# Optimization experiments

Hardware: AMD Instinct MI355X
Metric: run time of the kernel (lower is better)

The kernel has to match this reference:

```python
import jax, jax.numpy as jnp
from jax import lax
import numpy as np

B, T, IN, H, OUT = 1024, 512, 64, 128, 2
BN_EPS = 1e-5


def _gru_layer(x, w_ih, w_hh, b_ih, b_hh):
    # x: [B, T, F]; w_ih: [3H, F]; w_hh: [3H, H]; gate order = (r, z, n) as in PyTorch
    Bb = x.shape[0]
    Hh = w_hh.shape[1]
    xg = jnp.einsum('btf,gf->btg', x, w_ih) + b_ih  # precompute input gates [B, T, 3H]

    def step(h, xg_t):
        hg = h @ w_hh.T + b_hh                       # [B, 3H]
        xr, xz, xn = jnp.split(xg_t, 3, axis=-1)
        hr, hz, hn = jnp.split(hg, 3, axis=-1)
        r = jax.nn.sigmoid(xr + hr)
        z = jax.nn.sigmoid(xz + hz)
        n = jnp.tanh(xn + r * hn)
        h_new = (1.0 - z) * n + z * h
        return h_new, h_new

    h0 = jnp.zeros((Bb, Hh), dtype=x.dtype)
    _, ys = lax.scan(step, h0, jnp.swapaxes(xg, 0, 1))  # scan over time
    return jnp.swapaxes(ys, 0, 1)                        # [B, T, H]


def setup_inputs() -> dict:
    key = jax.random.key(0)
    ks = jax.random.split(key, 16)
    s_in = 1.0 / np.sqrt(H)  # PyTorch GRU init scale
    d = {
        'x': jax.random.normal(ks[0], (B, T, IN), dtype=jnp.float32),
        'w_ih0': jax.random.uniform(ks[1], (3 * H, IN), minval=-s_in, maxval=s_in),
        'w_hh0': jax.random.uniform(ks[2], (3 * H, H), minval=-s_in, maxval=s_in),
        'b_ih0': jax.random.uniform(ks[3], (3 * H,), minval=-s_in, maxval=s_in),
        'b_hh0': jax.random.uniform(ks[4], (3 * H,), minval=-s_in, maxval=s_in),
        'w_ih1': jax.random.uniform(ks[5], (3 * H, H), minval=-s_in, maxval=s_in),
        'w_hh1': jax.random.uniform(ks[6], (3 * H, H), minval=-s_in, maxval=s_in),
        'b_ih1': jax.random.uniform(ks[7], (3 * H,), minval=-s_in, maxval=s_in),
        'b_hh1': jax.random.uniform(ks[8], (3 * H,), minval=-s_in, maxval=s_in),
        'fc1_w': jax.random.normal(ks[9], (H // 2, H)) * 0.05,
        'fc1_b': jnp.zeros((H // 2,)),
        'fc2_w': jax.random.normal(ks[10], (OUT, H // 2)) * 0.05,
        'fc2_b': jnp.zeros((OUT,)),
        'bn_gamma': jnp.ones((H // 2,)),
        'bn_beta': jnp.zeros((H // 2,)),
        'bn_mean': jnp.zeros((H // 2,)),
        'bn_var': jnp.ones((H // 2,)),
    }
    return d


def reference(x, w_ih0, w_hh0, b_ih0, b_hh0, w_ih1, w_hh1, b_ih1, b_hh1,
              fc1_w, fc1_b, fc2_w, fc2_b, bn_gamma, bn_beta, bn_mean, bn_var):
    h1 = _gru_layer(x, w_ih0, w_hh0, b_ih0, b_hh0)   # [B, T, H]
    h2 = _gru_layer(h1, w_ih1, w_hh1, b_ih1, b_hh1)  # [B, T, H]
    out = h2[:, -1, :]                                # last timestep [B, H]
    # dropout = identity (eval mode)
    out = jax.nn.relu(out @ fc1_w.T + fc1_b)          # [B, H/2]
    out = (out - bn_mean) * jax.lax.rsqrt(bn_var + BN_EPS) * bn_gamma + bn_beta
    out = out @ fc2_w.T + fc2_b                       # [B, 2]
    return out
```

## Files before the change

### kernel.cpp

```cpp
#include <hip/hip_runtime.h>
#include <hip/hip_bf16.h>

namespace {

typedef _Float16 h16;
typedef _Float16 f16x8 __attribute__((ext_vector_type(8)));
typedef _Float16 f16x4 __attribute__((ext_vector_type(4)));
typedef _Float16 f16x2 __attribute__((ext_vector_type(2)));
typedef float    f32x4 __attribute__((ext_vector_type(4)));
typedef unsigned long long u64;

constexpr int T_SEQ = 512;
constexpr int B_SZ  = 1024;
constexpr int H_DIM = 128;
constexpr int ROWS  = 16;
constexpr int NT    = 512;
constexpr int NGRP  = B_SZ / ROWS;
constexpr int CHUNK = 32;

template <int INDIM, bool PROD>
__device__ void gru_body(char* smem_raw,
                         const float* __restrict__ xin,
                         const float* __restrict__ w_ih,
                         const float* __restrict__ w_hh,
                         const float* __restrict__ b_ih,
                         const float* __restrict__ b_hh,
                         u64* __restrict__ h1q,
                         int* __restrict__ flag,
                         float* __restrict__ h2out,
                         const int g)
{
  constexpr int KSH  = H_DIM / 32;
  constexpr int KSX  = INDIM / 32;
  constexpr int ROWP = H_DIM + INDIM + 8;

  auto hx = reinterpret_cast<h16 (*)[ROWS][ROWP]>(smem_raw);

  const int tid = threadIdx.x;
  const int wv  = tid >> 6;
  const int ln  = tid & 63;
  const int q   = ln >> 4;
  const int lr  = ln & 15;
  const int r0  = g * ROWS;
  const int j0  = wv * 16 + q * 4;

  f16x8 wA[3][KSH], wB[3][KSX];
  #pragma unroll
  for (int p = 0; p < 3; ++p) {
    const int gr = p * H_DIM + wv * 16 + lr;
    #pragma unroll
    for (int ks = 0; ks < KSH; ++ks) {
      const float* pw = w_hh + (size_t)gr * H_DIM + ks * 32 + q * 8;
      const float4 v0 = *(const float4*)(pw);
      const float4 v1 = *(const float4*)(pw + 4);
      f16x8 f;
      f[0]=(h16)v0.x; f[1]=(h16)v0.y; f[2]=(h16)v0.z; f[3]=(h16)v0.w;
      f[4]=(h16)v1.x; f[5]=(h16)v1.y; f[6]=(h16)v1.z; f[7]=(h16)v1.w;
      wA[p][ks] = f;
    }
    #pragma unroll
    for (int ks = 0; ks < KSX; ++ks) {
      const float* pw = w_ih + (size_t)gr * INDIM + ks * 32 + q * 8;
      const float4 v0 = *(const float4*)(pw);
      const float4 v1 = *(const float4*)(pw + 4);
      f16x8 f;
      f[0]=(h16)v0.x; f[1]=(h16)v0.y; f[2]=(h16)v0.z; f[3]=(h16)v0.w;
      f[4]=(h16)v1.x; f[5]=(h16)v1.y; f[6]=(h16)v1.z; f[7]=(h16)v1.w;
      wB[p][ks] = f;
    }
  }

  f32x4 bR, bZ, bNx, bNh;
  {
    const float4 ir  = *(const float4*)&b_ih[j0];
    const float4 hr  = *(const float4*)&b_hh[j0];
    const float4 iz  = *(const float4*)&b_ih[H_DIM + j0];
    const float4 hz  = *(const float4*)&b_hh[H_DIM + j0];
    const float4 in_ = *(const float4*)&b_ih[2 * H_DIM + j0];
    const float4 hn  = *(const float4*)&b_hh[2 * H_DIM + j0];
    bR[0]=ir.x+hr.x; bR[1]=ir.y+hr.y; bR[2]=ir.z+hr.z; bR[3]=ir.w+hr.w;
    bZ[0]=iz.x+hz.x; bZ[1]=iz.y+hz.y; bZ[2]=iz.z+hz.z; bZ[3]=iz.w+hz.w;
    bNx[0]=in_.x; bNx[1]=in_.y; bNx[2]=in_.z; bNx[3]=in_.w;
    bNh[0]=hn.x;  bNh[1]=hn.y;  bNh[2]=hn.z;  bNh[3]=hn.w;
  }

  const int sr = tid >> 5;
  const int si = tid & 31;

  {
    f16x4 z; z[0]=z[1]=z[2]=z[3] = (h16)0.f;
    *(f16x4*)&hx[0][sr][si * 4] = z;
  }
  f16x4 h_old; h_old[0]=h_old[1]=h_old[2]=h_old[3] = (h16)0.f;

  f16x2 sA, sB;
  if constexpr (PROD) {
    const float2 v0 = *(const float2*)(xin + ((size_t)(r0 + sr) * T_SEQ + 0) * 64 + si * 2);
    f16x2 s0; s0[0] = (h16)v0.x; s0[1] = (h16)v0.y;
    *(f16x2*)&hx[0][sr][H_DIM + si * 2] = s0;
    const float2 v1 = *(const float2*)(xin + ((size_t)(r0 + sr) * T_SEQ + 1) * 64 + si * 2);
    sA[0] = (h16)v1.x; sA[1] = (h16)v1.y;
  } else {
    while (__hip_atomic_load(flag, __ATOMIC_ACQUIRE, __HIP_MEMORY_SCOPE_AGENT) < 1)
      __builtin_amdgcn_s_sleep(2);
    const u64 bits = __hip_atomic_load(&h1q[((size_t)0 * B_SZ + r0 + sr) * 32 + si],
                                       __ATOMIC_RELAXED, __HIP_MEMORY_SCOPE_AGENT);
    f16x4 s0; __builtin_memcpy(&s0, &bits, 8);
    *(f16x4*)&hx[0][sr][H_DIM + si * 4] = s0;
  }
  __syncthreads();

  auto gates = [&](const f32x4& aR, const f32x4& aZ, const f32x4& aNx2, const f32x4& aNh2,
                   f16x4& nv4, float* hnv) {
    #pragma unroll
    for (int i = 0; i < 4; ++i) {
      const float rg = __builtin_amdgcn_rcpf(1.f + __expf(-aR[i]));
      const float zg = __builtin_amdgcn_rcpf(1.f + __expf(-aZ[i]));
      const float na = aNx2[i] + rg * aNh2[i];
      const float e2 = __expf(2.f * na);
      const float ng = 1.f - 2.f * __builtin_amdgcn_rcpf(e2 + 1.f);
      const float ho = (float)h_old[i];
      const float hn = ng + zg * (ho - ng);
      hnv[i] = hn;
      nv4[i] = (h16)hn;
    }
    h_old = nv4;
  };

  if constexpr (PROD) {
    auto pstep = [&](int t, int cur, f16x2& s_use, f16x2& s_load) {
      f16x8 bh[KSH], bx[KSX];
      #pragma unroll
      for (int ks = 0; ks < KSH; ++ks) bh[ks] = *(const f16x8*)&hx[cur][lr][ks * 32 + q * 8];
      #pragma unroll
      for (int ks = 0; ks < KSX; ++ks) bx[ks] = *(const f16x8*)&hx[cur][lr][H_DIM + ks * 32 + q * 8];

      {
        const int tt = (t + 2 < T_SEQ) ? t + 2 : T_SEQ - 1;
        const float2 v = *(const float2*)(xin + ((size_t)(r0 + sr) * T_SEQ + tt) * 64 + si * 2);
        s_load[0] = (h16)v.x; s_load[1] = (h16)v.y;
      }

      f32x4 aR = bR, aZ = bZ, aNh2 = bNh, aNx2 = bNx;
      #pragma unroll
      for (int ks = 0; ks < KSH; ++ks) {
        aR   = __builtin_amdgcn_mfma_f32_16x16x32_f16(wA[0][ks], bh[ks], aR, 0, 0, 0);
        aZ   = __builtin_amdgcn_mfma_f32_16x16x32_f16(wA[1][ks], bh[ks], aZ, 0, 0, 0);
        aNh2 = __builtin_amdgcn_mfma_f32_16x16x32_f16(wA[2][ks], bh[ks], aNh2, 0, 0, 0);
      }
      #pragma unroll
      for (int ks = 0; ks < KSX; ++ks) {
        aR   = __builtin_amdgcn_mfma_f32_16x16x32_f16(wB[0][ks], bx[ks], aR, 0, 0, 0);
        aZ   = __builtin_amdgcn_mfma_f32_16x16x32_f16(wB[1][ks], bx[ks], aZ, 0, 0, 0);
        aNx2 = __builtin_amdgcn_mfma_f32_16x16x32_f16(wB[2][ks], bx[ks], aNx2, 0, 0, 0);
      }

      f16x4 nv4; float hnv[4];
      gates(aR, aZ, aNx2, aNh2, nv4, hnv);

      u64 bits; __builtin_memcpy(&bits, &nv4, 8);
      __hip_atomic_store(&h1q[((size_t)t * B_SZ + r0 + lr) * 32 + (j0 >> 2)], bits,
                         __ATOMIC_RELAXED, __HIP_MEMORY_SCOPE_AGENT);

      *(f16x4*)&hx[cur ^ 1][lr][j0] = nv4;
      *(f16x2*)&hx[cur ^ 1][sr][H_DIM + si * 2] = s_use;

      if ((t & (CHUNK - 1)) == CHUNK - 1) __threadfence();
      __syncthreads();
      if (((t & (CHUNK - 1)) == CHUNK - 1) && tid == 0)
        __hip_atomic_store(flag, (t + 1) >> 5, __ATOMIC_RELEASE, __HIP_MEMORY_SCOPE_AGENT);
    };

    #pragma unroll 1
    for (int t = 0; t < T_SEQ; t += 2) {
      pstep(t,     0, sA, sB);
      pstep(t + 1, 1, sB, sA);
    }
  } else {
    #pragma unroll 1
    for (int t = 0; t < T_SEQ; ++t) {
      const int cur = t & 1;
      f16x8 bh[KSH], bx[KSX];
      #pragma unroll
      for (int ks = 0; ks < KSH; ++ks) bh[ks] = *(const f16x8*)&hx[cur][lr][ks * 32 + q * 8];
      #pragma unroll
      for (int ks = 0; ks < KSX; ++ks) bx[ks] = *(const f16x8*)&hx[cur][lr][H_DIM + ks * 32 + q * 8];

      f16x4 sN;
      const bool have = (t + 1 < T_SEQ);
      if (have) {
        if (((t + 1) & (CHUNK - 1)) == 0) {
          const int need = ((t + 1) >> 5) + 1;
          while (__hip_atomic_load(flag, __ATOMIC_ACQUIRE, __HIP_MEMORY_SCOPE_AGENT) < need)
            __builtin_amdgcn_s_sleep(2);
        }
        const u64 bits = __hip_atomic_load(&h1q[((size_t)(t + 1) * B_SZ + r0 + sr) * 32 + si],
                                           __ATOMIC_RELAXED, __HIP_MEMORY_SCOPE_AGENT);
        __builtin_memcpy(&sN, &bits, 8);
      }

      f32x4 aR = bR, aZ = bZ, aNh2 = bNh, aNx2 = bNx;
      #pragma unroll
      for (int ks = 0; ks < KSH; ++ks) {
        aR   = __builtin_amdgcn_mfma_f32_16x16x32_f16(wA[0][ks], bh[ks], aR, 0, 0, 0);
        aZ   = __builtin_amdgcn_mfma_f32_16x16x32_f16(wA[1][ks], bh[ks], aZ, 0, 0, 0);
        aNh2 = __builtin_amdgcn_mfma_f32_16x16x32_f16(wA[2][ks], bh[ks], aNh2, 0, 0, 0);
      }
      #pragma unroll
      for (int ks = 0; ks < KSX; ++ks) {
        aR   = __builtin_amdgcn_mfma_f32_16x16x32_f16(wB[0][ks], bx[ks], aR, 0, 0, 0);
        aZ   = __builtin_amdgcn_mfma_f32_16x16x32_f16(wB[1][ks], bx[ks], aZ, 0, 0, 0);
        aNx2 = __builtin_amdgcn_mfma_f32_16x16x32_f16(wB[2][ks], bx[ks], aNx2, 0, 0, 0);
      }

      f16x4 nv4; float hnv[4];
      gates(aR, aZ, aNx2, aNh2, nv4, hnv);

      *(f16x4*)&hx[cur ^ 1][lr][j0] = nv4;
      if (have) *(f16x4*)&hx[cur ^ 1][sr][H_DIM + si * 4] = sN;
      if (t == T_SEQ - 1)
        *(float4*)&h2out[(size_t)(r0 + lr) * H_DIM + j0] =
            make_float4(hnv[0], hnv[1], hnv[2], hnv[3]);
      __syncthreads();
    }
  }
}

__global__ __launch_bounds__(NT, 1)
void gru_fused(const float* __restrict__ x,
               const float* __restrict__ w_ih0, const float* __restrict__ w_hh0,
               const float* __restrict__ b_ih0, const float* __restrict__ b_hh0,
               const float* __restrict__ w_ih1, const float* __restrict__ w_hh1,
               const float* __restrict__ b_ih1, const float* __restrict__ b_hh1,
               u64* __restrict__ h1q, int* __restrict__ flags, float* __restrict__ h2)
{
  __shared__ __align__(16) char smem[(size_t)2 * ROWS * (H_DIM + H_DIM + 8) * sizeof(h16)];
  const int bid = blockIdx.x;
  if (bid < NGRP)
    gru_body<64, true>(smem, x, w_ih0, w_hh0, b_ih0, b_hh0, h1q, &flags[bid], nullptr, bid);
  else
    gru_body<128, false>(smem, nullptr, w_ih1, w_hh1, b_ih1, b_hh1, h1q,
                         &flags[bid - NGRP], h2, bid - NGRP);
}

__global__ __launch_bounds__(64)
void head_kernel(const float* __restrict__ h2,
                 const float* __restrict__ fc1_w, const float* __restrict__ fc1_b,
                 const float* __restrict__ fc2_w, const float* __restrict__ fc2_b,
                 const float* __restrict__ gamma, const float* __restrict__ beta,
                 const float* __restrict__ mean,  const float* __restrict__ var,
                 float* __restrict__ out)
{
  const int row = blockIdx.x;
  const int j   = threadIdx.x;
  __shared__ __align__(16) float hrow[H_DIM];
  __shared__ __align__(16) float act[64];

  hrow[j]      = h2[(size_t)row * H_DIM + j];
  hrow[64 + j] = h2[(size_t)row * H_DIM + 64 + j];
  __syncthreads();

  float s = fc1_b[j];
  const float4* wr = reinterpret_cast<const float4*>(fc1_w + (size_t)j * H_DIM);
  #pragma unroll
  for (int k4 = 0; k4 < H_DIM / 4; ++k4) {
    const float4 w = wr[k4];
    const float4 h = reinterpret_cast<const float4*>(hrow)[k4];
    s += w.x * h.x + w.y * h.y + w.z * h.z + w.w * h.w;
  }
  s = fmaxf(s, 0.f);
  s = (s - mean[j]) * rsqrtf(var[j] + 1e-5f) * gamma[j] + beta[j];
  act[j] = s;
  __syncthreads();

  if (j < 2) {
    float o = fc2_b[j];
    #pragma unroll
    for (int k = 0; k < 64; ++k) o += fc2_w[(size_t)j * 64 + k] * act[k];
    out[(size_t)row * 2 + j] = o;
  }
}

}

extern "C" void kernel_launch(void* const* d_in, const int* in_sizes, int n_in,
                              void* d_out, int out_size, void* d_ws, size_t ws_size,
                              hipStream_t stream) {
  const float* x     = (const float*)d_in[0];
  const float* w_ih0 = (const float*)d_in[1];
  const float* w_hh0 = (const float*)d_in[2];
  const float* b_ih0 = (const float*)d_in[3];
  const float* b_hh0 = (const float*)d_in[4];
  const float* w_ih1 = (const float*)d_in[5];
  const float* w_hh1 = (const float*)d_in[6];
  const float* b_ih1 = (const float*)d_in[7];
  const float* b_hh1 = (const float*)d_in[8];
  const float* fc1_w = (const float*)d_in[9];
  const float* fc1_b = (const float*)d_in[10];
  const float* fc2_w = (const float*)d_in[11];
  const float* fc2_b = (const float*)d_in[12];
  const float* gamma = (const float*)d_in[13];
  const float* beta  = (const float*)d_in[14];
  const float* mean  = (const float*)d_in[15];
  const float* var   = (const float*)d_in[16];
  float* out = (float*)d_out;

  char* ws = (char*)d_ws;
  const size_t h2_bytes = (size_t)B_SZ * H_DIM * sizeof(float);
  const size_t h1_bytes = (size_t)T_SEQ * B_SZ * H_DIM * sizeof(h16);
  const size_t fl_bytes = (size_t)NGRP * sizeof(int);
  if (ws_size < h2_bytes + h1_bytes + fl_bytes) return;

  float* h2    = (float*)ws;
  u64*   h1q   = (u64*)(ws + h2_bytes);
  int*   flags = (int*)(ws + h2_bytes + h1_bytes);

  hipMemsetAsync(flags, 0, fl_bytes, stream);
  gru_fused<<<dim3(2 * NGRP), dim3(NT), 0, stream>>>(
      x, w_ih0, w_hh0, b_ih0, b_hh0, w_ih1, w_hh1, b_ih1, b_hh1, h1q, flags, h2);
  head_kernel<<<dim3(B_SZ), dim3(64), 0, stream>>>(
      h2, fc1_w, fc1_b, fc2_w, fc2_b, gamma, beta, mean, var, out);
}
```

Before: 658.8 us.

## Store LDS operands in MFMA fragment order for conflict-free contiguous reads

New measurement: 747.2 us. 1.13x slower.

```diff
diff --git a/kernel.cpp b/kernel.cpp
--- a/kernel.cpp
+++ b/kernel.cpp
@@ -6,7 +6,6 @@
 typedef _Float16 h16;
 typedef _Float16 f16x8 __attribute__((ext_vector_type(8)));
 typedef _Float16 f16x4 __attribute__((ext_vector_type(4)));
-typedef _Float16 f16x2 __attribute__((ext_vector_type(2)));
 typedef float    f32x4 __attribute__((ext_vector_type(4)));
 typedef unsigned long long u64;
 
@@ -19,7 +18,7 @@
 constexpr int CHUNK = 32;
 
 template <int INDIM, bool PROD>
-__device__ void gru_body(char* smem_raw,
+__device__ void gru_body(h16* lds,
                          const float* __restrict__ xin,
                          const float* __restrict__ w_ih,
                          const float* __restrict__ w_hh,
@@ -30,11 +29,10 @@
                          float* __restrict__ h2out,
                          const int g)
 {
-  constexpr int KSH  = H_DIM / 32;
-  constexpr int KSX  = INDIM / 32;
-  constexpr int ROWP = H_DIM + INDIM + 8;
-
-  auto hx = reinterpret_cast<h16 (*)[ROWS][ROWP]>(smem_raw);
+  constexpr int CHH = H_DIM / 32;
+  constexpr int CXX = INDIM / 32;
+  constexpr int FH  = 0;
+  constexpr int FI  = 2 * CHH * 64;
 
   const int tid = threadIdx.x;
   const int wv  = tid >> 6;
@@ -44,30 +42,28 @@
   const int r0  = g * ROWS;
   const int j0  = wv * 16 + q * 4;
 
-  f16x8 wA[3][KSH], wB[3][KSX];
+  const int slotH = (wv >> 1) * 64 + ((wv & 1) * 2 + (q >> 1)) * 16 + lr;
+  const int e0    = (q & 1) * 4;
+
+  auto ldw = [](const float* pw) {
+    const float4 v0 = *(const float4*)(pw);
+    const float4 v1 = *(const float4*)(pw + 4);
+    f16x8 f;
+    f[0]=(h16)v0.x; f[1]=(h16)v0.y; f[2]=(h16)v0.z; f[3]=(h16)v0.w;
+    f[4]=(h16)v1.x; f[5]=(h16)v1.y; f[6]=(h16)v1.z; f[7]=(h16)v1.w;
+    return f;
+  };
+
+  f16x8 wA[3][CHH], wB[3][CXX];
   #pragma unroll
   for (int p = 0; p < 3; ++p) {
     const int gr = p * H_DIM + wv * 16 + lr;
     #pragma unroll
-    for (int ks = 0; ks < KSH; ++ks) {
-      const float* pw = w_hh + (size_t)gr * H_DIM + ks * 32 + q * 8;
-      const float4 v0 = *(const float4*)(pw);
-      const float4 v1 = *(const float4*)(pw + 4);
-      f16x8 f;
-      f[0]=(h16)v0.x; f[1]=(h16)v0.y; f[2]=(h16)v0.z; f[3]=(h16)v0.w;
-      f[4]=(h16)v1.x; f[5]=(h16)v1.y; f[6]=(h16)v1.z; f[7]=(h16)v1.w;
-      wA[p][ks] = f;
-    }
-    #pragma unroll
-    for (int ks = 0; ks < KSX; ++ks) {
-      const float* pw = w_ih + (size_t)gr * INDIM + ks * 32 + q * 8;
-      const float4 v0 = *(const float4*)(pw);
-      const float4 v1 = *(const float4*)(pw + 4);
-      f16x8 f;
-      f[0]=(h16)v0.x; f[1]=(h16)v0.y; f[2]=(h16)v0.z; f[3]=(h16)v0.w;
-      f[4]=(h16)v1.x; f[5]=(h16)v1.y; f[6]=(h16)v1.z; f[7]=(h16)v1.w;
-      wB[p][ks] = f;
-    }
+    for (int ks = 0; ks < CHH; ++ks)
+      wA[p][ks] = ldw(w_hh + (size_t)gr * H_DIM + ks * 32 + q * 8);
+    #pragma unroll
+    for (int ks = 0; ks < CXX; ++ks)
+      wB[p][ks] = ldw(w_ih + (size_t)gr * INDIM + ks * 32 + q * 8);
   }
 
   f32x4 bR, bZ, bNx, bNh;
@@ -84,29 +80,50 @@
     bNh[0]=hn.x;  bNh[1]=hn.y;  bNh[2]=hn.z;  bNh[3]=hn.w;
   }
 
-  const int sr = tid >> 5;
-  const int si = tid & 31;
+  auto rd = [&](int cb) { return *(const f16x8*)&lds[(cb + ln) * 8]; };
+
+  const int  sc  = (tid >> 6) & 3;
+  const int  sl  = tid & 63;
+  const bool stg = (tid < CXX * 64);
+  const size_t xrow = (size_t)(r0 + (sl & 15)) * T_SEQ;
+  const int    xk   = (sl >> 4) * 8 + sc * 32;
+
+  auto load_x = [&](int t, f16x8& d) {
+    if (stg) {
+      const float* p = xin + (xrow + t) * 64 + xk;
+      const float4 v0 = *(const float4*)(p);
+      const float4 v1 = *(const float4*)(p + 4);
+      d[0]=(h16)v0.x; d[1]=(h16)v0.y; d[2]=(h16)v0.z; d[3]=(h16)v0.w;
+      d[4]=(h16)v1.x; d[5]=(h16)v1.y; d[6]=(h16)v1.z; d[7]=(h16)v1.w;
+    }
+  };
+  auto load_h1 = [&](int t, f16x8& d) {
+    if (stg) {
+      const size_t base = ((size_t)t * B_SZ + r0 + (sl & 15)) * 32 + sc * 8 + (sl >> 4) * 2;
+      const u64 b0 = __hip_atomic_load(&h1q[base],     __ATOMIC_RELAXED, __HIP_MEMORY_SCOPE_AGENT);
+      const u64 b1 = __hip_atomic_load(&h1q[base + 1], __ATOMIC_RELAXED, __HIP_MEMORY_SCOPE_AGENT);
+      __builtin_memcpy(&d,                  &b0, 8);
+      __builtin_memcpy((char*)&d + 8,       &b1, 8);
+    }
+  };
+  auto stage_in = [&](int buf, const f16x8& s) {
+    if (stg) *(f16x8*)&lds[(FI + buf * CXX * 64 + sc * 64 + sl) * 8] = s;
+  };
 
   {
-    f16x4 z; z[0]=z[1]=z[2]=z[3] = (h16)0.f;
-    *(f16x4*)&hx[0][sr][si * 4] = z;
+    f16x8 z; z[0]=z[1]=z[2]=z[3]=z[4]=z[5]=z[6]=z[7] = (h16)0.f;
+    if (tid < 2 * CHH * 64 / 2) *(f16x8*)&lds[(FH + tid % 256) * 8] = z;
   }
   f16x4 h_old; h_old[0]=h_old[1]=h_old[2]=h_old[3] = (h16)0.f;
 
-  f16x2 sA, sB;
+  f16x8 sA, sB;
   if constexpr (PROD) {
-    const float2 v0 = *(const float2*)(xin + ((size_t)(r0 + sr) * T_SEQ + 0) * 64 + si * 2);
-    f16x2 s0; s0[0] = (h16)v0.x; s0[1] = (h16)v0.y;
-    *(f16x2*)&hx[0][sr][H_DIM + si * 2] = s0;
-    const float2 v1 = *(const float2*)(xin + ((size_t)(r0 + sr) * T_SEQ + 1) * 64 + si * 2);
-    sA[0] = (h16)v1.x; sA[1] = (h16)v1.y;
+    f16x8 s0; load_x(0, s0); stage_in(0, s0);
+    load_x(1, sA);
   } else {
     while (__hip_atomic_load(flag, __ATOMIC_ACQUIRE, __HIP_MEMORY_SCOPE_AGENT) < 1)
       __builtin_amdgcn_s_sleep(2);
-    const u64 bits = __hip_atomic_load(&h1q[((size_t)0 * B_SZ + r0 + sr) * 32 + si],
-                                       __ATOMIC_RELAXED, __HIP_MEMORY_SCOPE_AGENT);
-    f16x4 s0; __builtin_memcpy(&s0, &bits, 8);
-    *(f16x4*)&hx[0][sr][H_DIM + si * 4] = s0;
+    f16x8 s0; load_h1(0, s0); stage_in(0, s0);
   }
   __syncthreads();
 
@@ -127,33 +144,35 @@
     h_old = nv4;
   };
 
+  auto mfma_all = [&](const f16x8* bh, const f16x8* bx,
+                      f32x4& aR, f32x4& aZ, f32x4& aNh2, f32x4& aNx2) {
+    aR = bR; aZ = bZ; aNh2 = bNh; aNx2 = bNx;
+    #pragma unroll
+    for (int ks = 0; ks < CHH; ++ks) {
+      aR   = __builtin_amdgcn_mfma_f32_16x16x32_f16(wA[0][ks], bh[ks], aR, 0, 0, 0);
+      aZ   = __builtin_amdgcn_mfma_f32_16x16x32_f16(wA[1][ks], bh[ks], aZ, 0, 0, 0);
+      aNh2 = __builtin_amdgcn_mfma_f32_16x16x32_f16(wA[2][ks], bh[ks], aNh2, 0, 0, 0);
+    }
+    #pragma unroll
+    for (int ks = 0; ks < CXX; ++ks) {
+      aR   = __builtin_amdgcn_mfma_f32_16x16x32_f16(wB[0][ks], bx[ks], aR, 0, 0, 0);
+      aZ   = __builtin_amdgcn_mfma_f32_16x16x32_f16(wB[1][ks], bx[ks], aZ, 0, 0, 0);
+      aNx2 = __builtin_amdgcn_mfma_f32_16x16x32_f16(wB[2][ks], bx[ks], aNx2, 0, 0, 0);
+    }
+  };
+
   if constexpr (PROD) {
-    auto pstep = [&](int t, int cur, f16x2& s_use, f16x2& s_load) {
-      f16x8 bh[KSH], bx[KSX];
+    auto pstep = [&](int t, int cur, f16x8& s_use, f16x8& s_load) {
+      f16x8 bh[CHH], bx[CXX];
       #pragma unroll
-      for (int ks = 0; ks < KSH; ++ks) bh[ks] = *(const f16x8*)&hx[cur][lr][ks * 32 + q * 8];
+      for (int ks = 0; ks < CHH; ++ks) bh[ks] = rd(FH + cur * CHH * 64 + ks * 64);
       #pragma unroll
-      for (int ks = 0; ks < KSX; ++ks) bx[ks] = *(const f16x8*)&hx[cur][lr][H_DIM + ks * 32 + q * 8];
-
-      {
-        const int tt = (t + 2 < T_SEQ) ? t + 2 : T_SEQ - 1;
-        const float2 v = *(const float2*)(xin + ((size_t)(r0 + sr) * T_SEQ + tt) * 64 + si * 2);
-        s_load[0] = (h16)v.x; s_load[1] = (h16)v.y;
-      }
-
-      f32x4 aR = bR, aZ = bZ, aNh2 = bNh, aNx2 = bNx;
-      #pragma unroll
-      for (int ks = 0; ks < KSH; ++ks) {
-        aR   = __builtin_amdgcn_mfma_f32_16x16x32_f16(wA[0][ks], bh[ks], aR, 0, 0, 0);
-        aZ   = __builtin_amdgcn_mfma_f32_16x16x32_f16(wA[1][ks], bh[ks], aZ, 0, 0, 0);
-        aNh2 = __builtin_amdgcn_mfma_f32_16x16x32_f16(wA[2][ks], bh[ks], aNh2, 0, 0, 0);
-      }
-      #pragma unroll
-      for (int ks = 0; ks < KSX; ++ks) {
-        aR   = __builtin_amdgcn_mfma_f32_16x16x32_f16(wB[0][ks], bx[ks], aR, 0, 0, 0);
-        aZ   = __builtin_amdgcn_mfma_f32_16x16x32_f16(wB[1][ks], bx[ks], aZ, 0, 0, 0);
-        aNx2 = __builtin_amdgcn_mfma_f32_16x16x32_f16(wB[2][ks], bx[ks], aNx2, 0, 0, 0);
-      }
+      for (int ks = 0; ks < CXX; ++ks) bx[ks] = rd(FI + cur * CXX * 64 + ks * 64);
+
+      load_x((t + 2 < T_SEQ) ? t + 2 : T_SEQ - 1, s_load);
+
+      f32x4 aR, aZ, aNh2, aNx2;
+      mfma_all(bh, bx, aR, aZ, aNh2, aNx2);
 
       f16x4 nv4; float hnv[4];
       gates(aR, aZ, aNx2, aNh2, nv4, hnv);
@@ -162,13 +181,13 @@
       __hip_atomic_store(&h1q[((size_t)t * B_SZ + r0 + lr) * 32 + (j0 >> 2)], bits,
                          __ATOMIC_RELAXED, __HIP_MEMORY_SCOPE_AGENT);
 
-      *(f16x4*)&hx[cur ^ 1][lr][j0] = nv4;
-      *(f16x2*)&hx[cur ^ 1][sr][H_DIM + si * 2] = s_use;
+      *(f16x4*)&lds[(FH + (cur ^ 1) * CHH * 64 + slotH) * 8 + e0] = nv4;
+      stage_in(cur ^ 1, s_use);
 
       if ((t & (CHUNK - 1)) == CHUNK - 1) __threadfence();
       __syncthreads();
       if (((t & (CHUNK - 1)) == CHUNK - 1) && tid == 0)
-        __hip_atomic_store(flag, (t + 1) >> 5, __ATOMIC_RELEASE, __HIP_MEMORY_SCOPE_AGENT);
+        __hip_atomic_store(flag, (t + 1) / CHUNK, __ATOMIC_RELEASE, __HIP_MEMORY_SCOPE_AGENT);
     };
 
     #pragma unroll 1
@@ -180,44 +199,31 @@
     #pragma unroll 1
     for (int t = 0; t < T_SEQ; ++t) {
       const int cur = t & 1;
-      f16x8 bh[KSH], bx[KSX];
+      f16x8 bh[CHH], bx[CXX];
       #pragma unroll
-      for (int ks = 0; ks < KSH; ++ks) bh[ks] = *(const f16x8*)&hx[cur][lr][ks * 32 + q * 8];
+      for (int ks = 0; ks < CHH; ++ks) bh[ks] = rd(FH + cur * CHH * 64 + ks * 64);
       #pragma unroll
-      for (int ks = 0; ks < KSX; ++ks) bx[ks] = *(const f16x8*)&hx[cur][lr][H_DIM + ks * 32 + q * 8];
-
-      f16x4 sN;
+      for (int ks = 0; ks < CXX; ++ks) bx[ks] = rd(FI + cur * CXX * 64 + ks * 64);
+
+      f16x8 sN;
       const bool have = (t + 1 < T_SEQ);
       if (have) {
         if (((t + 1) & (CHUNK - 1)) == 0) {
-          const int need = ((t + 1) >> 5) + 1;
+          const int need = (t + 1) / CHUNK + 1;
           while (__hip_atomic_load(flag, __ATOMIC_ACQUIRE, __HIP_MEMORY_SCOPE_AGENT) < need)
             __builtin_amdgcn_s_sleep(2);
         }
-        const u64 bits = __hip_atomic_load(&h1q[((size_t)(t + 1) * B_SZ + r0 + sr) * 32 + si],
-                                           __ATOMIC_RELAXED, __HIP_MEMORY_SCOPE_AGENT);
-        __builtin_memcpy(&sN, &bits, 8);
+        load_h1(t + 1, sN);
       }
 
-      f32x4 aR = bR, aZ = bZ, aNh2 = bNh, aNx2 = bNx;
-      #pragma unroll
-      for (int ks = 0; ks < KSH; ++ks) {
-        aR   = __builtin_amdgcn_mfma_f32_16x16x32_f16(wA[0][ks], bh[ks], aR, 0, 0, 0);
-        aZ   = __builtin_amdgcn_mfma_f32_16x16x32_f16(wA[1][ks], bh[ks], aZ, 0, 0, 0);
-        aNh2 = __builtin_amdgcn_mfma_f32_16x16x32_f16(wA[2][ks], bh[ks], aNh2, 0, 0, 0);
-      }
-      #pragma unroll
-      for (int ks = 0; ks < KSX; ++ks) {
-        aR   = __builtin_amdgcn_mfma_f32_16x16x32_f16(wB[0][ks], bx[ks], aR, 0, 0, 0);
-        aZ   = __builtin_amdgcn_mfma_f32_16x16x32_f16(wB[1][ks], bx[ks], aZ, 0, 0, 0);
-        aNx2 = __builtin_amdgcn_mfma_f32_16x16x32_f16(wB[2][ks], bx[ks], aNx2, 0, 0, 0);
-      }
+      f32x4 aR, aZ, aNh2, aNx2;
+      mfma_all(bh, bx, aR, aZ, aNh2, aNx2);
 
       f16x4 nv4; float hnv[4];
       gates(aR, aZ, aNx2, aNh2, nv4, hnv);
 
-      *(f16x4*)&hx[cur ^ 1][lr][j0] = nv4;
-      if (have) *(f16x4*)&hx[cur ^ 1][sr][H_DIM + si * 4] = sN;
+      *(f16x4*)&lds[(FH + (cur ^ 1) * CHH * 64 + slotH) * 8 + e0] = nv4;
+      if (have) stage_in(cur ^ 1, sN);
       if (t == T_SEQ - 1)
         *(float4*)&h2out[(size_t)(r0 + lr) * H_DIM + j0] =
             make_float4(hnv[0], hnv[1], hnv[2], hnv[3]);
@@ -234,12 +240,12 @@
                const float* __restrict__ b_ih1, const float* __restrict__ b_hh1,
                u64* __restrict__ h1q, int* __restrict__ flags, float* __restrict__ h2)
 {
-  __shared__ __align__(16) char smem[(size_t)2 * ROWS * (H_DIM + H_DIM + 8) * sizeof(h16)];
+  __shared__ __align__(16) h16 lds[1024 * 8];
   const int bid = blockIdx.x;
   if (bid < NGRP)
-    gru_body<64, true>(smem, x, w_ih0, w_hh0, b_ih0, b_hh0, h1q, &flags[bid], nullptr, bid);
+    gru_body<64, true>(lds, x, w_ih0, w_hh0, b_ih0, b_hh0, h1q, &flags[bid], nullptr, bid);
   else
-    gru_body<128, false>(smem, nullptr, w_ih1, w_hh1, b_ih1, b_hh1, h1q,
+    gru_body<128, false>(lds, nullptr, w_ih1, w_hh1, b_ih1, b_hh1, h1q,
                          &flags[bid - NGRP], h2, bid - NGRP);
 }
 
```

## Fuse MLP head into GRU consumer blocks and prefetch layer-1 input two steps ahead

Applied to the files above, without the earlier changes.

New measurement: 663.7 us. No clear change (+0.7%).

```diff
diff --git a/kernel.cpp b/kernel.cpp
--- a/kernel.cpp
+++ b/kernel.cpp
@@ -19,7 +19,7 @@
 constexpr int CHUNK = 32;
 
 template <int INDIM, bool PROD>
-__device__ void gru_body(char* smem_raw,
+__device__ void gru_body(char* smem_raw, float* headbuf,
                          const float* __restrict__ xin,
                          const float* __restrict__ w_ih,
                          const float* __restrict__ w_hh,
@@ -27,7 +27,15 @@
                          const float* __restrict__ b_hh,
                          u64* __restrict__ h1q,
                          int* __restrict__ flag,
-                         float* __restrict__ h2out,
+                         const float* __restrict__ fc1_w,
+                         const float* __restrict__ fc1_b,
+                         const float* __restrict__ fc2_w,
+                         const float* __restrict__ fc2_b,
+                         const float* __restrict__ gamma,
+                         const float* __restrict__ beta,
+                         const float* __restrict__ mean,
+                         const float* __restrict__ var,
+                         float* __restrict__ out,
                          const int g)
 {
   constexpr int KSH  = H_DIM / 32;
@@ -93,7 +101,14 @@
   }
   f16x4 h_old; h_old[0]=h_old[1]=h_old[2]=h_old[3] = (h16)0.f;
 
+  auto load_h1 = [&](int t, f16x4& d) {
+    const u64 bits = __hip_atomic_load(&h1q[((size_t)t * B_SZ + r0 + sr) * 32 + si],
+                                       __ATOMIC_RELAXED, __HIP_MEMORY_SCOPE_AGENT);
+    __builtin_memcpy(&d, &bits, 8);
+  };
+
   f16x2 sA, sB;
+  f16x4 cA, cB;
   if constexpr (PROD) {
     const float2 v0 = *(const float2*)(xin + ((size_t)(r0 + sr) * T_SEQ + 0) * 64 + si * 2);
     f16x2 s0; s0[0] = (h16)v0.x; s0[1] = (h16)v0.y;
@@ -103,10 +118,9 @@
   } else {
     while (__hip_atomic_load(flag, __ATOMIC_ACQUIRE, __HIP_MEMORY_SCOPE_AGENT) < 1)
       __builtin_amdgcn_s_sleep(2);
-    const u64 bits = __hip_atomic_load(&h1q[((size_t)0 * B_SZ + r0 + sr) * 32 + si],
-                                       __ATOMIC_RELAXED, __HIP_MEMORY_SCOPE_AGENT);
-    f16x4 s0; __builtin_memcpy(&s0, &bits, 8);
+    f16x4 s0; load_h1(0, s0);
     *(f16x4*)&hx[0][sr][H_DIM + si * 4] = s0;
+    load_h1(1, cA);
   }
   __syncthreads();
 
@@ -127,6 +141,23 @@
     h_old = nv4;
   };
 
+  auto mfma_all = [&](const f16x8* bh, const f16x8* bx,
+                      f32x4& aR, f32x4& aZ, f32x4& aNh2, f32x4& aNx2) {
+    aR = bR; aZ = bZ; aNh2 = bNh; aNx2 = bNx;
+    #pragma unroll
+    for (int ks = 0; ks < KSH; ++ks) {
+      aR   = __builtin_amdgcn_mfma_f32_16x16x32_f16(wA[0][ks], bh[ks], aR, 0, 0, 0);
+      aZ   = __builtin_amdgcn_mfma_f32_16x16x32_f16(wA[1][ks], bh[ks], aZ, 0, 0, 0);
+      aNh2 = __builtin_amdgcn_mfma_f32_16x16x32_f16(wA[2][ks], bh[ks], aNh2, 0, 0, 0);
+    }
+    #pragma unroll
+    for (int ks = 0; ks < KSX; ++ks) {
+      aR   = __builtin_amdgcn_mfma_f32_16x16x32_f16(wB[0][ks], bx[ks], aR, 0, 0, 0);
+      aZ   = __builtin_amdgcn_mfma_f32_16x16x32_f16(wB[1][ks], bx[ks], aZ, 0, 0, 0);
+      aNx2 = __builtin_amdgcn_mfma_f32_16x16x32_f16(wB[2][ks], bx[ks], aNx2, 0, 0, 0);
+    }
+  };
+
   if constexpr (PROD) {
     auto pstep = [&](int t, int cur, f16x2& s_use, f16x2& s_load) {
       f16x8 bh[KSH], bx[KSX];
@@ -141,19 +172,8 @@
         s_load[0] = (h16)v.x; s_load[1] = (h16)v.y;
       }
 
-      f32x4 aR = bR, aZ = bZ, aNh2 = bNh, aNx2 = bNx;
-      #pragma unroll
-      for (int ks = 0; ks < KSH; ++ks) {
-        aR   = __builtin_amdgcn_mfma_f32_16x16x32_f16(wA[0][ks], bh[ks], aR, 0, 0, 0);
-        aZ   = __builtin_amdgcn_mfma_f32_16x16x32_f16(wA[1][ks], bh[ks], aZ, 0, 0, 0);
-        aNh2 = __builtin_amdgcn_mfma_f32_16x16x32_f16(wA[2][ks], bh[ks], aNh2, 0, 0, 0);
-      }
-      #pragma unroll
-      for (int ks = 0; ks < KSX; ++ks) {
-        aR   = __builtin_amdgcn_mfma_f32_16x16x32_f16(wB[0][ks], bx[ks], aR, 0, 0, 0);
-        aZ   = __builtin_amdgcn_mfma_f32_16x16x32_f16(wB[1][ks], bx[ks], aZ, 0, 0, 0);
-        aNx2 = __builtin_amdgcn_mfma_f32_16x16x32_f16(wB[2][ks], bx[ks], aNx2, 0, 0, 0);
-      }
+      f32x4 aR, aZ, aNh2, aNx2;
+      mfma_all(bh, bx, aR, aZ, aNh2, aNx2);
 
       f16x4 nv4; float hnv[4];
       gates(aR, aZ, aNx2, aNh2, nv4, hnv);
@@ -168,7 +188,7 @@
       if ((t & (CHUNK - 1)) == CHUNK - 1) __threadfence();
       __syncthreads();
       if (((t & (CHUNK - 1)) == CHUNK - 1) && tid == 0)
-        __hip_atomic_store(flag, (t + 1) >> 5, __ATOMIC_RELEASE, __HIP_MEMORY_SCOPE_AGENT);
+        __hip_atomic_store(flag, (t + 1) / CHUNK, __ATOMIC_RELEASE, __HIP_MEMORY_SCOPE_AGENT);
     };
 
     #pragma unroll 1
@@ -177,51 +197,72 @@
       pstep(t + 1, 1, sB, sA);
     }
   } else {
-    #pragma unroll 1
-    for (int t = 0; t < T_SEQ; ++t) {
-      const int cur = t & 1;
+    auto cstep = [&](int t, int cur, f16x4& s_use, f16x4& s_load) {
       f16x8 bh[KSH], bx[KSX];
       #pragma unroll
       for (int ks = 0; ks < KSH; ++ks) bh[ks] = *(const f16x8*)&hx[cur][lr][ks * 32 + q * 8];
       #pragma unroll
       for (int ks = 0; ks < KSX; ++ks) bx[ks] = *(const f16x8*)&hx[cur][lr][H_DIM + ks * 32 + q * 8];
 
-      f16x4 sN;
-      const bool have = (t + 1 < T_SEQ);
-      if (have) {
-        if (((t + 1) & (CHUNK - 1)) == 0) {
-          const int need = ((t + 1) >> 5) + 1;
+      if (t + 2 < T_SEQ) {
+        if (((t + 2) & (CHUNK - 1)) == 0) {
+          const int need = (t + 2) / CHUNK + 1;
           while (__hip_atomic_load(flag, __ATOMIC_ACQUIRE, __HIP_MEMORY_SCOPE_AGENT) < need)
             __builtin_amdgcn_s_sleep(2);
         }
-        const u64 bits = __hip_atomic_load(&h1q[((size_t)(t + 1) * B_SZ + r0 + sr) * 32 + si],
-                                           __ATOMIC_RELAXED, __HIP_MEMORY_SCOPE_AGENT);
-        __builtin_memcpy(&sN, &bits, 8);
+        load_h1(t + 2, s_load);
       }
 
-      f32x4 aR = bR, aZ = bZ, aNh2 = bNh, aNx2 = bNx;
-      #pragma unroll
-      for (int ks = 0; ks < KSH; ++ks) {
-        aR   = __builtin_amdgcn_mfma_f32_16x16x32_f16(wA[0][ks], bh[ks], aR, 0, 0, 0);
-        aZ   = __builtin_amdgcn_mfma_f32_16x16x32_f16(wA[1][ks], bh[ks], aZ, 0, 0, 0);
-        aNh2 = __builtin_amdgcn_mfma_f32_16x16x32_f16(wA[2][ks], bh[ks], aNh2, 0, 0, 0);
-      }
-      #pragma unroll
-      for (int ks = 0; ks < KSX; ++ks) {
-        aR   = __builtin_amdgcn_mfma_f32_16x16x32_f16(wB[0][ks], bx[ks], aR, 0, 0, 0);
-        aZ   = __builtin_amdgcn_mfma_f32_16x16x32_f16(wB[1][ks], bx[ks], aZ, 0, 0, 0);
-        aNx2 = __builtin_amdgcn_mfma_f32_16x16x32_f16(wB[2][ks], bx[ks], aNx2, 0, 0, 0);
-      }
+      f32x4 aR, aZ, aNh2, aNx2;
+      mfma_all(bh, bx, aR, aZ, aNh2, aNx2);
 
       f16x4 nv4; float hnv[4];
       gates(aR, aZ, aNx2, aNh2, nv4, hnv);
 
       *(f16x4*)&hx[cur ^ 1][lr][j0] = nv4;
-      if (have) *(f16x4*)&hx[cur ^ 1][sr][H_DIM + si * 4] = sN;
-      if (t == T_SEQ - 1)
-        *(float4*)&h2out[(size_t)(r0 + lr) * H_DIM + j0] =
-            make_float4(hnv[0], hnv[1], hnv[2], hnv[3]);
+      if (t + 1 < T_SEQ) *(f16x4*)&hx[cur ^ 1][sr][H_DIM + si * 4] = s_use;
+
+      if (t == T_SEQ - 1) {
+        float* h2f = headbuf;
+        float* act = headbuf + 16 * 128;
+        #pragma unroll
+        for (int i = 0; i < 4; ++i) h2f[lr * 128 + j0 + i] = hnv[i];
+        __syncthreads();
+        {
+          const int row = tid >> 5;
+          const float* hr = &h2f[row * 128];
+          #pragma unroll
+          for (int half = 0; half < 2; ++half) {
+            const int j = (tid & 31) + half * 32;
+            float s = fc1_b[j];
+            const float4* wr = (const float4*)(fc1_w + (size_t)j * H_DIM);
+            #pragma unroll
+            for (int k4 = 0; k4 < H_DIM / 4; ++k4) {
+              const float4 w = wr[k4];
+              const float4 h = ((const float4*)hr)[k4];
+              s += w.x * h.x + w.y * h.y + w.z * h.z + w.w * h.w;
+            }
+            s = fmaxf(s, 0.f);
+            s = (s - mean[j]) * rsqrtf(var[j] + 1e-5f) * gamma[j] + beta[j];
+            act[row * 64 + j] = s;
+          }
+        }
+        __syncthreads();
+        if (tid < 32) {
+          const int r = tid >> 1, o = tid & 1;
+          float s = fc2_b[o];
+          #pragma unroll
+          for (int k = 0; k < 64; ++k) s += fc2_w[(size_t)o * 64 + k] * act[r * 64 + k];
+          out[(size_t)(r0 + r) * 2 + o] = s;
+        }
+      }
       __syncthreads();
+    };
+
+    #pragma unroll 1
+    for (int t = 0; t < T_SEQ; t += 2) {
+      cstep(t,     0, cA, cB);
+      cstep(t + 1, 1, cB, cA);
     }
   }
 }
@@ -232,53 +273,24 @@
                const float* __restrict__ b_ih0, const float* __restrict__ b_hh0,
                const float* __restrict__ w_ih1, const float* __restrict__ w_hh1,
                const float* __restrict__ b_ih1, const float* __restrict__ b_hh1,
-               u64* __restrict__ h1q, int* __restrict__ flags, float* __restrict__ h2)
+               u64* __restrict__ h1q, int* __restrict__ flags,
+               const float* __restrict__ fc1_w, const float* __restrict__ fc1_b,
+               const float* __restrict__ fc2_w, const float* __restrict__ fc2_b,
+               const float* __restrict__ gamma, const float* __restrict__ beta,
+               const float* __restrict__ mean,  const float* __restrict__ var,
+               float* __restrict__ out)
 {
   __shared__ __align__(16) char smem[(size_t)2 * ROWS * (H_DIM + H_DIM + 8) * sizeof(h16)];
+  __shared__ __align__(16) float headbuf[16 * 128 + 16 * 64];
   const int bid = blockIdx.x;
   if (bid < NGRP)
-    gru_body<64, true>(smem, x, w_ih0, w_hh0, b_ih0, b_hh0, h1q, &flags[bid], nullptr, bid);
+    gru_body<64, true>(smem, headbuf, x, w_ih0, w_hh0, b_ih0, b_hh0, h1q, &flags[bid],
+                       nullptr, nullptr, nullptr, nullptr, nullptr, nullptr, nullptr, nullptr,
+                       nullptr, bid);
   else
-    gru_body<128, false>(smem, nullptr, w_ih1, w_hh1, b_ih1, b_hh1, h1q,
-                         &flags[bid - NGRP], h2, bid - NGRP);
-}
-
-__global__ __launch_bounds__(64)
-void head_kernel(const float* __restrict__ h2,
-                 const float* __restrict__ fc1_w, const float* __restrict__ fc1_b,
-                 const float* __restrict__ fc2_w, const float* __restrict__ fc2_b,
-                 const float* __restrict__ gamma, const float* __restrict__ beta,
-                 const float* __restrict__ mean,  const float* __restrict__ var,
-                 float* __restrict__ out)
-{
-  const int row = blockIdx.x;
-  const int j   = threadIdx.x;
-  __shared__ __align__(16) float hrow[H_DIM];
-  __shared__ __align__(16) float act[64];
-
-  hrow[j]      = h2[(size_t)row * H_DIM + j];
-  hrow[64 + j] = h2[(size_t)row * H_DIM + 64 + j];
-  __syncthreads();
-
-  float s = fc1_b[j];
-  const float4* wr = reinterpret_cast<const float4*>(fc1_w + (size_t)j * H_DIM);
-  #pragma unroll
-  for (int k4 = 0; k4 < H_DIM / 4; ++k4) {
-    const float4 w = wr[k4];
-    const float4 h = reinterpret_cast<const float4*>(hrow)[k4];
-    s += w.x * h.x + w.y * h.y + w.z * h.z + w.w * h.w;
-  }
-  s = fmaxf(s, 0.f);
-  s = (s - mean[j]) * rsqrtf(var[j] + 1e-5f) * gamma[j] + beta[j];
-  act[j] = s;
-  __syncthreads();
-
-  if (j < 2) {
-    float o = fc2_b[j];
-    #pragma unroll
-    for (int k = 0; k < 64; ++k) o += fc2_w[(size_t)j * 64 + k] * act[k];
-    out[(size_t)row * 2 + j] = o;
-  }
+    gru_body<128, false>(smem, headbuf, nullptr, w_ih1, w_hh1, b_ih1, b_hh1, h1q,
+                         &flags[bid - NGRP], fc1_w, fc1_b, fc2_w, fc2_b, gamma, beta,
+                         mean, var, out, bid - NGRP);
 }
 
 }
@@ -306,18 +318,15 @@
   float* out = (float*)d_out;
 
   char* ws = (char*)d_ws;
-  const size_t h2_bytes = (size_t)B_SZ * H_DIM * sizeof(float);
   const size_t h1_bytes = (size_t)T_SEQ * B_SZ * H_DIM * sizeof(h16);
   const size_t fl_bytes = (size_t)NGRP * sizeof(int);
-  if (ws_size < h2_bytes + h1_bytes + fl_bytes) return;
-
-  float* h2    = (float*)ws;
-  u64*   h1q   = (u64*)(ws + h2_bytes);
-  int*   flags = (int*)(ws + h2_bytes + h1_bytes);
+  if (ws_size < h1_bytes + fl_bytes) return;
+
+  u64* h1q   = (u64*)ws;
+  int* flags = (int*)(ws + h1_bytes);
 
   hipMemsetAsync(flags, 0, fl_bytes, stream);
   gru_fused<<<dim3(2 * NGRP), dim3(NT), 0, stream>>>(
-      x, w_ih0, w_hh0, b_ih0, b_hh0, w_ih1, w_hh1, b_ih1, b_hh1, h1q, flags, h2);
-  head_kernel<<<dim3(B_SZ), dim3(64), 0, stream>>>(
-      h2, fc1_w, fc1_b, fc2_w, fc2_b, gamma, beta, mean, var, out);
+      x, w_ih0, w_hh0, b_ih0, b_hh0, w_ih1, w_hh1, b_ih1, b_hh1, h1q, flags,
+      fc1_w, fc1_b, fc2_w, fc2_b, gamma, beta, mean, var, out);
 }
```
